# Performance work log

Measured on AMD Instinct MI355X. Metric: run time of the kernel, lower is better.

## Reference

```python
import jax, jax.numpy as jnp
import numpy as np

N, E, IN, HID, OUT, H, NCLS = 20000, 320000, 128, 32, 8, 8, 10

def _ln(x, g, b, eps=1e-5):
    mu = x.mean(-1, keepdims=True)
    var = ((x - mu) ** 2).mean(-1, keepdims=True)
    return g * (x - mu) / jnp.sqrt(var + eps) + b

def _gelu(x):
    return jax.nn.gelu(x, approximate=False)

def _tconv(x, src, dst, Wq, bq, Wk, bk, Wv, bv, Ws, bs, heads):
    # PyG TransformerConv, concat=True, root_weight=True, lin_beta is None
    n = x.shape[0]
    C = Wq.shape[1] // heads
    q = (x @ Wq + bq).reshape(n, heads, C)
    k = (x @ Wk + bk).reshape(n, heads, C)
    v = (x @ Wv + bv).reshape(n, heads, C)
    logits = (q[dst] * k[src]).sum(-1) / jnp.sqrt(jnp.asarray(C, x.dtype))  # [E,H]
    m = jax.lax.stop_gradient(jax.ops.segment_max(logits, dst, num_segments=n))
    e = jnp.exp(logits - m[dst])
    denom = jax.ops.segment_sum(e, dst, num_segments=n)
    alpha = e / (denom[dst] + 1e-16)  # per-target-node edge softmax
    agg = jax.ops.segment_sum(alpha[:, :, None] * v[src], dst, num_segments=n)
    out = agg.reshape(n, heads * C) + x @ Ws + bs
    return out, alpha

def _forward(src, dst, x,
             c1_Wq, c1_bq, c1_Wk, c1_bk, c1_Wv, c1_bv, c1_Ws, c1_bs,
             c2_Wq, c2_bq, c2_Wk, c2_bk, c2_Wv, c2_bv, c2_Ws, c2_bs,
             c3_Wq, c3_bq, c3_Wk, c3_bk, c3_Wv, c3_bv, c3_Ws, c3_bs,
             c4_Wq, c4_bq, c4_Wk, c4_bk, c4_Wv, c4_bv, c4_Ws, c4_bs,
             n1_g, n1_b, n2_g, n2_b, n3_g, n3_b, n4_g, n4_b,
             fc_W, fc_b):
    h1 = _ln(_gelu(_tconv(x, src, dst, c1_Wq, c1_bq, c1_Wk, c1_bk, c1_Wv, c1_bv, c1_Ws, c1_bs, H)[0]), n1_g, n1_b)
    h2_raw, attn = _tconv(h1, src, dst, c2_Wq, c2_bq, c2_Wk, c2_bk, c2_Wv, c2_bv, c2_Ws, c2_bs, H)
    h2 = _ln(_gelu(h2_raw), n2_g, n2_b)
    h3 = _ln(_gelu(_tconv(h2, src, dst, c3_Wq, c3_bq, c3_Wk, c3_bk, c3_Wv, c3_bv, c3_Ws, c3_bs, H)[0]), n3_g, n3_b)
    h4 = _ln(_gelu(_tconv(h3, src, dst, c4_Wq, c4_bq, c4_Wk, c4_bk, c4_Wv, c4_bv, c4_Ws, c4_bs, 1)[0]), n4_g, n4_b)
    x_out = h2 @ fc_W + fc_b
    return x_out, h4, attn

def setup_inputs() -> dict:
    key = jax.random.key(0)
    ks = iter(jax.random.split(key, 64))
    def p(shape, s=0.05):
        return jax.random.normal(next(ks), shape, dtype=jnp.float32) * s
    inp = {}
    inp['x'] = jax.random.normal(next(ks), (N, IN), dtype=jnp.float32)
    inp['edge_index'] = jax.random.randint(next(ks), (2, E), 0, N, dtype=jnp.int32)
    dims = [('c1', IN, H * HID), ('c2', H * HID, H * OUT), ('c3', H * OUT, H * HID), ('c4', H * HID, IN)]
    for name, di, do in dims:
        for w in ['Wq', 'Wk', 'Wv', 'Ws']:
            inp[name + '_' + w] = p((di, do))
        for bnm in ['bq', 'bk', 'bv', 'bs']:
            inp[name + '_' + bnm] = jnp.zeros((do,), jnp.float32)
    for nm, d in [('n1', H * HID), ('n2', H * OUT), ('n3', H * HID), ('n4', IN)]:
        inp[nm + '_g'] = jnp.ones((d,), jnp.float32)
        inp[nm + '_b'] = jnp.zeros((d,), jnp.float32)
    inp['fc_W'] = p((H * OUT, NCLS))
    inp['fc_b'] = jnp.zeros((NCLS,), jnp.float32)
    return inp

def reference(x, edge_index,
              c1_Wq, c1_bq, c1_Wk, c1_bk, c1_Wv, c1_bv, c1_Ws, c1_bs,
              c2_Wq, c2_bq, c2_Wk, c2_bk, c2_Wv, c2_bv, c2_Ws, c2_bs,
              c3_Wq, c3_bq, c3_Wk, c3_bk, c3_Wv, c3_bv, c3_Ws, c3_bs,
              c4_Wq, c4_bq, c4_Wk, c4_bk, c4_Wv, c4_bv, c4_Ws, c4_bs,
              n1_g, n1_b, n2_g, n2_b, n3_g, n3_b, n4_g, n4_b,
              fc_W, fc_b):
    src, dst = edge_index[0], edge_index[1]
    return _forward(src, dst, x,
                    c1_Wq, c1_bq, c1_Wk, c1_bk, c1_Wv, c1_bv, c1_Ws, c1_bs,
                    c2_Wq, c2_bq, c2_Wk, c2_bk, c2_Wv, c2_bv, c2_Ws, c2_bs,
                    c3_Wq, c3_bq, c3_Wk, c3_bk, c3_Wv, c3_bv, c3_Ws, c3_bs,
                    c4_Wq, c4_bq, c4_Wk, c4_bk, c4_Wv, c4_bv, c4_Ws, c4_bs,
                    n1_g, n1_b, n2_g, n2_b, n3_g, n3_b, n4_g, n4_b,
                    fc_W, fc_b)
```

## Files before the change

kernel.cpp:

```cpp
#include <hip/hip_runtime.h>
#include <hip/hip_bf16.h>
#include <math.h>

#define NN 20000
#define MP 20032
#define NE 320000

typedef __hip_bfloat16 bf16;
typedef __attribute__((ext_vector_type(8))) short short8v;
typedef __attribute__((ext_vector_type(4))) short short4v;
typedef __attribute__((ext_vector_type(4))) float f32x4;

__device__ __forceinline__ float b2f(bf16 v){ return __bfloat162float(v); }
__device__ __forceinline__ bf16 f2b(float v){ return __float2bfloat16(v); }
__device__ __forceinline__ float bfbits(short s){
  return __uint_as_float(((unsigned)(unsigned short)s) << 16);
}
__device__ __forceinline__ int clampi(int v, int lo, int hi){ return v < lo ? lo : (v > hi ? hi : v); }
__device__ __forceinline__ void stv(bf16* p, float v){ *p = f2b(v); }
__device__ __forceinline__ void stv(float* p, float v){ *p = v; }
__device__ __forceinline__ float ldv(const bf16* p){ return b2f(*p); }
__device__ __forceinline__ float ldv(const float* p){ return *p; }

__device__ __forceinline__ float fast_erf(float x){
  float ax = fabsf(x);
  float t = __builtin_amdgcn_rcpf(1.f + 0.3275911f*ax);
  float p = ((((1.061405429f*t - 1.453152027f)*t + 1.421413741f)*t
              - 0.284496736f)*t + 0.254829592f)*t;
  float y = 1.f - p*__expf(-ax*ax);
  return copysignf(y, x);
}
__device__ __forceinline__ float gelu(float x){
  return 0.5f*x*(1.f + fast_erf(x*0.70710678118654752f));
}

template<int CPL>
__device__ __forceinline__ void ldrow(const bf16* p, float* o){
  if constexpr (CPL == 16){
    short8v v0 = *reinterpret_cast<const short8v*>(p);
    short8v v1 = *reinterpret_cast<const short8v*>(p + 8);
#pragma unroll
    for (int j = 0; j < 8; j++){ o[j] = bfbits(v0[j]); o[8+j] = bfbits(v1[j]); }
  } else if constexpr (CPL == 8){
    short8v v = *reinterpret_cast<const short8v*>(p);
#pragma unroll
    for (int j = 0; j < 8; j++) o[j] = bfbits(v[j]);
  } else {
    short4v v = *reinterpret_cast<const short4v*>(p);
#pragma unroll
    for (int j = 0; j < 4; j++) o[j] = bfbits(v[j]);
  }
}
template<int CPL>
__device__ __forceinline__ void ldrowT(const bf16* p, float* o){ ldrow<CPL>(p, o); }
template<int CPL>
__device__ __forceinline__ void ldrowT(const float* p, float* o){
#pragma unroll
  for (int j = 0; j < CPL; j += 4){
    float4 v = *reinterpret_cast<const float4*>(p + j);
    o[j] = v.x; o[j+1] = v.y; o[j+2] = v.z; o[j+3] = v.w;
  }
}

__device__ __forceinline__ short8v ldA8(const bf16* p){
  return *reinterpret_cast<const short8v*>(p);
}
__device__ __forceinline__ short8v ldA8(const float* p){
  float4 a0 = *reinterpret_cast<const float4*>(p);
  float4 a1 = *reinterpret_cast<const float4*>(p + 4);
  short8v r;
  bf16 b;
  b = f2b(a0.x); r[0] = *(const short*)&b;
  b = f2b(a0.y); r[1] = *(const short*)&b;
  b = f2b(a0.z); r[2] = *(const short*)&b;
  b = f2b(a0.w); r[3] = *(const short*)&b;
  b = f2b(a1.x); r[4] = *(const short*)&b;
  b = f2b(a1.y); r[5] = *(const short*)&b;
  b = f2b(a1.z); r[6] = *(const short*)&b;
  b = f2b(a1.w); r[7] = *(const short*)&b;
  return r;
}

__global__ void fill_k(float* __restrict__ out, int n, float val){
  int i = blockIdx.x*blockDim.x + threadIdx.x;
  if (i < n) out[i] = val;
}

struct PackArgs {
  const float* w[16];
  unsigned long long off[16];
  int K[16];
  int D[16];
};
__global__ void pack_all(PackArgs pa, bf16* __restrict__ out){
  int wi = blockIdx.y;
  int K = pa.K[wi], D = pa.D[wi];
  int i = blockIdx.x*256 + threadIdx.x;
  if (i >= K*D) return;
  int j = i & 7, l = (i >> 3) & 63;
  int TG = D >> 4;
  int tg = (i >> 9) % TG, s = (i >> 9) / TG;
  int k = s*32 + (l >> 4)*8 + j, n = tg*16 + (l & 15);
  out[pa.off[wi] + i] = f2b(pa.w[wi][(size_t)k*D + n]);
}

template<typename AT, typename TS>
__global__ void gemm_qkvs(const AT* __restrict__ X,
    const short8v* __restrict__ WQ, const short8v* __restrict__ WK,
    const short8v* __restrict__ WV, const short8v* __restrict__ WS,
    const float* __restrict__ bQ, const float* __restrict__ bK,
    const float* __restrict__ bV, const float* __restrict__ bS,
    bf16* __restrict__ Qo, bf16* __restrict__ Ko, bf16* __restrict__ Vo,
    TS* __restrict__ So,
    int K, int TG, int ldQ, int ldKV, int ldS, int MstoreS){
  int w = threadIdx.x >> 6, lane = threadIdx.x & 63;
  int n0 = blockIdx.x*64;
  size_t m0 = (size_t)blockIdx.y*64 + w*16;
  int lr = lane & 15, lk = lane >> 4;
  int ar = clampi((int)(m0 + lr), 0, NN-1);
  const AT* xp = X + (size_t)ar*K + lk*8;
  size_t wo = ((size_t)(n0 >> 4))*64 + lane;
  f32x4 acc[4][4];
#pragma unroll
  for (int j = 0; j < 4; j++)
#pragma unroll
    for (int t = 0; t < 4; t++) acc[j][t] = f32x4{0,0,0,0};
  int steps = K >> 5;
  for (int s = 0; s < steps; s++){
    short8v a = ldA8(xp + s*32);
    size_t ro = wo + (size_t)s*TG*64;
#pragma unroll
    for (int t = 0; t < 4; t++){
      size_t idx = ro + t*64;
      acc[0][t] = __builtin_amdgcn_mfma_f32_16x16x32_bf16(a, WQ[idx], acc[0][t], 0, 0, 0);
      acc[1][t] = __builtin_amdgcn_mfma_f32_16x16x32_bf16(a, WK[idx], acc[1][t], 0, 0, 0);
      acc[2][t] = __builtin_amdgcn_mfma_f32_16x16x32_bf16(a, WV[idx], acc[2][t], 0, 0, 0);
      acc[3][t] = __builtin_amdgcn_mfma_f32_16x16x32_bf16(a, WS[idx], acc[3][t], 0, 0, 0);
    }
  }
#pragma unroll
  for (int t = 0; t < 4; t++){
    int col = n0 + t*16 + lr;
    float b0 = bQ[col], b1 = bK[col], b2 = bV[col], b3 = bS[col];
#pragma unroll
    for (int r = 0; r < 4; r++){
      size_t row = m0 + lk*4 + r;
      Qo[row*(size_t)ldQ  + col] = f2b(acc[0][t][r] + b0);
      Ko[row*(size_t)ldKV + col] = f2b(acc[1][t][r] + b1);
      Vo[row*(size_t)ldKV + col] = f2b(acc[2][t][r] + b2);
      if ((int)row < MstoreS) stv(&So[row*(size_t)ldS + col], acc[3][t][r] + b3);
    }
  }
}

__global__ void count_k(const int* __restrict__ ei, int* __restrict__ cnt, int E){
  int e = blockIdx.x*blockDim.x + threadIdx.x;
  if (e < E){
    int d = clampi(ei[E + e], 0, NN-1);
    atomicAdd(&cnt[d], 1);
  }
}

__global__ void exscan_k(const int* __restrict__ cnt, int* __restrict__ off,
                         int* __restrict__ cur, int n){
  __shared__ int wtot[16];
  __shared__ int carrysh;
  int tid = threadIdx.x, lane = tid & 63, w = tid >> 6;
  if (tid == 0) carrysh = 0;
  __syncthreads();
  for (int base = 0; base < n; base += 1024){
    int i = base + tid;
    int v = (i < n) ? cnt[i] : 0;
    int s = v;
#pragma unroll
    for (int d = 1; d < 64; d <<= 1){
      int t = __shfl_up(s, d);
      if (lane >= d) s += t;
    }
    if (lane == 63) wtot[w] = s;
    __syncthreads();
    int woff = 0;
    for (int j = 0; j < w; j++) woff += wtot[j];
    int c = carrysh;
    if (i < n){ int val = c + woff + s - v; off[i] = val; cur[i] = val; }
    __syncthreads();
    if (tid == 1023) carrysh = c + woff + s;
    __syncthreads();
  }
  if (threadIdx.x == 0) off[n] = carrysh;
}

__global__ void scatter_k(const int* __restrict__ ei, int* __restrict__ cur,
                          int* __restrict__ perm, int* __restrict__ srcs, int E){
  int e = blockIdx.x*blockDim.x + threadIdx.x;
  if (e >= E) return;
  int s = clampi(ei[e], 0, NN-1);
  int d = clampi(ei[E + e], 0, NN-1);
  int p = atomicAdd(&cur[d], 1);
  if (p >= 0 && p < E){ perm[p] = e; srcs[p] = s; }
}

template<int D, int H, typename TO>
__global__ void fused_attn(const bf16* __restrict__ Q, const bf16* __restrict__ KV,
                           const int* __restrict__ srcs, const int* __restrict__ offs,
                           TO* __restrict__ Xout, int ldO,
                           const float* __restrict__ G, const float* __restrict__ Bt,
                           bf16* __restrict__ LOG, const int* __restrict__ perm,
                           float* __restrict__ attn_out, float scale){
  constexpr int CPL = D/16;
  constexpr int LPH = 16/H;
  int node = blockIdx.x*4 + (threadIdx.x >> 6);
  if (node >= NN) return;
  int lane = threadIdx.x & 63;
  int hl = lane & 15;
  int slot = lane >> 4;
  float q[CPL];
  {
    float tmp[CPL];
    ldrow<CPL>(Q + (size_t)node*D + hl*CPL, tmp);
#pragma unroll
    for (int j = 0; j < CPL; j++) q[j] = tmp[j] * scale;
  }
  float den = 0.f;
  float acc[CPL];
#pragma unroll
  for (int j = 0; j < CPL; j++) acc[j] = 0.f;
  int s0 = offs[node], e0 = offs[node+1];

  float kA[CPL], vA[CPL], kB[CPL], vB[CPL];
  auto LD = [&](int i, float* k, float* v){
    int sc = (i < e0) ? srcs[i] : 0;
    const bf16* base = KV + (size_t)sc*(2*D) + hl*CPL;
    ldrow<CPL>(base,     k);
    ldrow<CPL>(base + D, v);
  };
  auto PROC = [&](int i, const float* k, const float* v){
    float t = 0.f;
#pragma unroll
    for (int j = 0; j < CPL; j++) t += q[j]*k[j];
#pragma unroll
    for (int o = 1; o < LPH; o <<= 1) t += __shfl_xor(t, o);
    bool val = i < e0;
    if (LOG && val && ((hl & (LPH-1)) == 0)) LOG[(size_t)i*H + hl/LPH] = f2b(t);
    float pe = val ? __expf(t) : 0.f;
    den += pe;
#pragma unroll
    for (int j = 0; j < CPL; j++) acc[j] += pe*v[j];
  };

  int iA = s0 + slot;
  int iters = (e0 - s0 + 3) >> 2;
  LD(iA, kA, vA);
  for (int it = 0; it < iters; it += 2){
    LD(iA + 4, kB, vB);
    PROC(iA, kA, vA);
    LD(iA + 8, kA, vA);
    PROC(iA + 4, kB, vB);
    iA += 8;
  }
  den += __shfl_xor(den, 16);
  den += __shfl_xor(den, 32);
#pragma unroll
  for (int j = 0; j < CPL; j++){
    acc[j] += __shfl_xor(acc[j], 16);
    acc[j] += __shfl_xor(acc[j], 32);
  }
  float inv = 1.f/(den + 1e-16f);

  {
    float sk[CPL];
    ldrowT<CPL>(Xout + (size_t)node*ldO + hl*CPL, sk);
    float v[CPL]; float s = 0.f;
#pragma unroll
    for (int j = 0; j < CPL; j++){
      float ge = gelu(sk[j] + acc[j]*inv);
      v[j] = ge; s += ge;
    }
#pragma unroll
    for (int o = 1; o < 16; o <<= 1) s += __shfl_xor(s, o);
    float mu = s * (1.f/D);
    float qv = 0.f;
#pragma unroll
    for (int j = 0; j < CPL; j++){ float d2 = v[j]-mu; qv += d2*d2; }
#pragma unroll
    for (int o = 1; o < 16; o <<= 1) qv += __shfl_xor(qv, o);
    float lni = 1.f / sqrtf(qv*(1.f/D) + 1e-5f);
    if (slot == 0){
      TO* oo = Xout + (size_t)node*ldO + hl*CPL;
#pragma unroll
      for (int j = 0; j < CPL; j++){
        int c = hl*CPL + j;
        stv(&oo[j], G[c]*(v[j]-mu)*lni + Bt[c]);
      }
    }
  }

  if (attn_out){
    asm volatile("s_waitcnt vmcnt(0)" ::: "memory");
    int total = (e0 - s0) * H;
    int it2 = (total + 63) >> 6;
    for (int b = 0; b < it2; b++){
      int idx = b*64 + lane;
      int h = idx & (H-1);
      float dh = __shfl(den, h*LPH);
      if (idx < total){
        int pos = s0 + (idx >> 3);
        float lg = b2f(LOG[(size_t)pos*H + h]);
        attn_out[(size_t)perm[pos]*H + h] = __expf(lg)/(dh + 1e-16f);
      }
    }
  }
}

__global__ void fc_k(const bf16* __restrict__ X, const float* __restrict__ W,
                     const float* __restrict__ B, float* __restrict__ Out,
                     int K, int D){
  int m = blockIdx.x*4 + (threadIdx.x >> 6);
  int lane = threadIdx.x & 63;
  if (m >= NN || lane >= D) return;
  float acc = B[lane];
  for (int k = 0; k < K; k++) acc += b2f(X[(size_t)m*K + k]) * W[(size_t)k*D + lane];
  Out[(size_t)m*D + lane] = acc;
}

extern "C" void kernel_launch(void* const* d_in, const int* in_sizes, int n_in,
                              void* d_out, int out_size, void* d_ws, size_t ws_size,
                              hipStream_t stream){
  int code = 0;
  if (n_in != 44) code = 100;
  else {
    const int wsz[4] = {32768,16384,16384,32768};
    const int bsz[4] = {256,64,256,128};
    bool ok = in_sizes[0] == NN*128 && in_sizes[1] == 2*NE
           && in_sizes[42] == 640 && in_sizes[43] == 10;
    for (int l = 0; l < 4 && ok; l++){
      for (int j = 0; j < 4; j++)
        ok = ok && in_sizes[2+l*8+j] == wsz[l] && in_sizes[2+l*8+4+j] == bsz[l];
      ok = ok && in_sizes[34+2*l] == bsz[l] && in_sizes[35+2*l] == bsz[l];
    }
    if (!ok) code = 140;
  }
  if (code){
    fill_k<<<((size_t)out_size+255)/256, 256, 0, stream>>>((float*)d_out, out_size, (float)code);
    return;
  }

  const float* x = (const float*)d_in[0];
  const int*   ei = (const int*)d_in[1];
  const float *W[4][4], *Bw[4][4], *lng[4], *lnb[4];
  for (int l = 0; l < 4; l++){
    for (int j = 0; j < 4; j++){
      W[l][j]  = (const float*)d_in[2 + l*8 + j];
      Bw[l][j] = (const float*)d_in[2 + l*8 + 4 + j];
    }
    lng[l] = (const float*)d_in[34 + 2*l];
    lnb[l] = (const float*)d_in[35 + 2*l];
  }
  const float* fcW = (const float*)d_in[42];
  const float* fcB = (const float*)d_in[43];

  char* ws = (char*)d_ws;
  size_t o = 0;
  auto alloc = [&](size_t bytes)->void*{ void* p = ws + o; o += (bytes + 255)/256*256; return p; };
  bf16* Hb   = (bf16*)alloc((size_t)MP*256*2);
  bf16* H2b  = (bf16*)alloc((size_t)MP*64*2);
  bf16* Qb   = (bf16*)alloc((size_t)MP*256*2);
  bf16* KVb  = (bf16*)alloc((size_t)MP*512*2);
  bf16* LOG  = (bf16*)alloc((size_t)NE*8*2);
  int* OFFS  = (int*)alloc((size_t)(NN+1)*4);
  int* CNT   = (int*)alloc((size_t)(NN+1)*4);
  int* CURS  = (int*)alloc((size_t)(NN+1)*4);
  int* PERM  = (int*)alloc((size_t)NE*4);
  int* SRCS  = (int*)alloc((size_t)(NE+16)*4);
  bf16* WPK  = (bf16*)alloc((size_t)393216*2);
  size_t need = o;

  float* out_x  = (float*)d_out;
  float* out_h4 = out_x + (size_t)NN*10;
  float* out_at = out_h4 + (size_t)NN*128;

  if (ws_size < need){
    fill_k<<<((size_t)out_size+255)/256, 256, 0, stream>>>((float*)d_out, out_size, 160.0f);
    return;
  }

  const int KD[4] = {128,256,64,256};
  const int DD[4] = {256,64,256,128};
  PackArgs pa;
  bf16* Wp[4][4];
  {
    size_t off = 0;
    for (int l = 0; l < 4; l++)
      for (int j = 0; j < 4; j++){
        int idx = l*4 + j;
        pa.w[idx] = W[l][j];
        pa.off[idx] = off;
        pa.K[idx] = KD[l];
        pa.D[idx] = DD[l];
        Wp[l][j] = WPK + off;
        off += (size_t)KD[l]*DD[l];
      }
  }
  pack_all<<<dim3(128,16),256,0,stream>>>(pa, WPK);

  hipMemsetAsync(CNT, 0, (size_t)NN*4, stream);
  count_k<<<NE/256, 256, 0, stream>>>(ei, CNT, NE);
  exscan_k<<<1, 1024, 0, stream>>>(CNT, OFFS, CURS, NN);
  scatter_k<<<NE/256, 256, 0, stream>>>(ei, CURS, PERM, SRCS, NE);

  const float s32  = 0.1767766952966369f;
  const float s8   = 0.3535533905932738f;
  const float s128 = 0.0883883476483184f;
  const dim3 g64(1, MP/64), g128(2, MP/64), g256(4, MP/64);

  gemm_qkvs<float,bf16><<<g256,256,0,stream>>>(x,
      (const short8v*)Wp[0][0], (const short8v*)Wp[0][1],
      (const short8v*)Wp[0][2], (const short8v*)Wp[0][3],
      Bw[0][0], Bw[0][1], Bw[0][2], Bw[0][3],
      Qb, KVb, KVb + 256, Hb, 128, 16, 256, 512, 256, MP);
  fused_attn<256,8,bf16><<<NN/4,256,0,stream>>>(Qb, KVb, SRCS, OFFS, Hb, 256,
      lng[0], lnb[0], nullptr, nullptr, nullptr, s32);

  gemm_qkvs<bf16,bf16><<<g64,256,0,stream>>>(Hb,
      (const short8v*)Wp[1][0], (const short8v*)Wp[1][1],
      (const short8v*)Wp[1][2], (const short8v*)Wp[1][3],
      Bw[1][0], Bw[1][1], Bw[1][2], Bw[1][3],
      Qb, KVb, KVb + 64, H2b, 256, 4, 64, 128, 64, MP);
  fused_attn<64,8,bf16><<<NN/4,256,0,stream>>>(Qb, KVb, SRCS, OFFS, H2b, 64,
      lng[1], lnb[1], LOG, PERM, out_at, s8);

  fc_k<<<NN/4,256,0,stream>>>(H2b, fcW, fcB, out_x, 64, 10);

  gemm_qkvs<bf16,bf16><<<g256,256,0,stream>>>(H2b,
      (const short8v*)Wp[2][0], (const short8v*)Wp[2][1],
      (const short8v*)Wp[2][2], (const short8v*)Wp[2][3],
      Bw[2][0], Bw[2][1], Bw[2][2], Bw[2][3],
      Qb, KVb, KVb + 256, Hb, 64, 16, 256, 512, 256, MP);
  fused_attn<256,8,bf16><<<NN/4,256,0,stream>>>(Qb, KVb, SRCS, OFFS, Hb, 256,
      lng[2], lnb[2], nullptr, nullptr, nullptr, s32);

  gemm_qkvs<bf16,float><<<g128,256,0,stream>>>(Hb,
      (const short8v*)Wp[3][0], (const short8v*)Wp[3][1],
      (const short8v*)Wp[3][2], (const short8v*)Wp[3][3],
      Bw[3][0], Bw[3][1], Bw[3][2], Bw[3][3],
      Qb, KVb, KVb + 128, out_h4, 256, 8, 128, 256, 128, NN);
  fused_attn<128,1,float><<<NN/4,256,0,stream>>>(Qb, KVb, SRCS, OFFS, out_h4, 128,
      lng[3], lnb[3], nullptr, nullptr, nullptr, s128);
}
```

Baseline: 340.6 us.

## Split wide attention layers into head-group blocks with separate GELU+LayerNorm pass

For the two 256-wide TransformerConv layers, the attention aggregation is split across a second grid dimension of 4 head groups. Each wave now handles 64 channels (4 per lane) instead of 256, which cuts registers per lane and raises occupancy and parallelism. GELU and LayerNorm, which need the whole row, move into a separate gelu_ln kernel, at the cost of an extra launch and an extra read/write of the hidden buffer. The edge loop in fused_attn is also changed from a two-buffer unrolled prefetch to a simpler single-step prefetch with register rotation.

New measurement: 349.6 us. 1.03x slower.

```diff
diff --git a/kernel.cpp b/kernel.cpp
--- a/kernel.cpp
+++ b/kernel.cpp
@@ -30,7 +30,7 @@
   float y = 1.f - p*__expf(-ax*ax);
   return copysignf(y, x);
 }
-__device__ __forceinline__ float gelu(float x){
+__device__ __forceinline__ float gelu_f(float x){
   return 0.5f*x*(1.f + fast_erf(x*0.70710678118654752f));
 }
 
@@ -200,6 +200,108 @@
   if (p >= 0 && p < E){ perm[p] = e; srcs[p] = s; }
 }
 
+template<int D, int H, int NHG>
+__global__ void attn_hg(const bf16* __restrict__ Q, const bf16* __restrict__ KV,
+                        const int* __restrict__ srcs, const int* __restrict__ offs,
+                        bf16* __restrict__ Xout, float scale){
+  constexpr int DG  = D/NHG;
+  constexpr int CPL = DG/16;
+  constexpr int LPH = (D/H)/CPL;
+  int node = blockIdx.x*4 + (threadIdx.x >> 6);
+  if (node >= NN) return;
+  int cb = blockIdx.y*DG;
+  int lane = threadIdx.x & 63;
+  int hl = lane & 15;
+  int slot = lane >> 4;
+  float q[CPL];
+  {
+    float tmp[CPL];
+    ldrow<CPL>(Q + (size_t)node*D + cb + hl*CPL, tmp);
+#pragma unroll
+    for (int j = 0; j < CPL; j++) q[j] = tmp[j] * scale;
+  }
+  float den = 0.f;
+  float acc[CPL];
+#pragma unroll
+  for (int j = 0; j < CPL; j++) acc[j] = 0.f;
+  int s0 = offs[node], e0 = offs[node+1];
+  int i = s0 + slot;
+  bool vcur = i < e0;
+  int sc = vcur ? srcs[i] : 0;
+  float kc[CPL], vc[CPL];
+  {
+    const bf16* base = KV + (size_t)sc*(2*D) + cb + hl*CPL;
+    ldrow<CPL>(base, kc); ldrow<CPL>(base + D, vc);
+  }
+  int iters = (e0 - s0 + 3) >> 2;
+  for (int it = 0; it < iters; ++it){
+    int inext = i + 4;
+    bool vnxt = inext < e0;
+    int sn = vnxt ? srcs[inext] : 0;
+    float kn[CPL], vn[CPL];
+    {
+      const bf16* base = KV + (size_t)sn*(2*D) + cb + hl*CPL;
+      ldrow<CPL>(base, kn); ldrow<CPL>(base + D, vn);
+    }
+    float t = 0.f;
+#pragma unroll
+    for (int j = 0; j < CPL; j++) t += q[j]*kc[j];
+#pragma unroll
+    for (int o = 1; o < LPH; o <<= 1) t += __shfl_xor(t, o);
+    float pe = vcur ? __expf(t) : 0.f;
+    den += pe;
+#pragma unroll
+    for (int j = 0; j < CPL; j++) acc[j] += pe*vc[j];
+    vcur = vnxt; i = inext;
+#pragma unroll
+    for (int j = 0; j < CPL; j++){ kc[j] = kn[j]; vc[j] = vn[j]; }
+  }
+  den += __shfl_xor(den, 16);
+  den += __shfl_xor(den, 32);
+#pragma unroll
+  for (int j = 0; j < CPL; j++){
+    acc[j] += __shfl_xor(acc[j], 16);
+    acc[j] += __shfl_xor(acc[j], 32);
+  }
+  float inv = 1.f/(den + 1e-16f);
+  if (slot == 0){
+    bf16* oo = Xout + (size_t)node*D + cb + hl*CPL;
+#pragma unroll
+    for (int j = 0; j < CPL; j++) oo[j] = f2b(b2f(oo[j]) + acc[j]*inv);
+  }
+}
+
+template<int CPL>
+__global__ void gelu_ln(bf16* __restrict__ X, const float* __restrict__ G,
+                        const float* __restrict__ Bt){
+  int node = blockIdx.x*4 + (threadIdx.x >> 6);
+  if (node >= NN) return;
+  constexpr int D = CPL*64;
+  int lane = threadIdx.x & 63;
+  bf16* xr = X + (size_t)node*D + lane*CPL;
+  float v[CPL]; float s = 0.f;
+  {
+    float tmp[CPL];
+    ldrow<CPL>(xr, tmp);
+#pragma unroll
+    for (int j = 0; j < CPL; j++){ float ge = gelu_f(tmp[j]); v[j] = ge; s += ge; }
+  }
+#pragma unroll
+  for (int off = 1; off < 64; off <<= 1) s += __shfl_xor(s, off);
+  float mu = s * (1.f/D);
+  float q = 0.f;
+#pragma unroll
+  for (int j = 0; j < CPL; j++){ float d = v[j]-mu; q += d*d; }
+#pragma unroll
+  for (int off = 1; off < 64; off <<= 1) q += __shfl_xor(q, off);
+  float inv = 1.f / sqrtf(q*(1.f/D) + 1e-5f);
+#pragma unroll
+  for (int j = 0; j < CPL; j++){
+    int c = lane*CPL + j;
+    xr[j] = f2b(G[c]*(v[j]-mu)*inv + Bt[c]);
+  }
+}
+
 template<int D, int H, typename TO>
 __global__ void fused_attn(const bf16* __restrict__ Q, const bf16* __restrict__ KV,
                            const int* __restrict__ srcs, const int* __restrict__ offs,
@@ -226,37 +328,37 @@
 #pragma unroll
   for (int j = 0; j < CPL; j++) acc[j] = 0.f;
   int s0 = offs[node], e0 = offs[node+1];
-
-  float kA[CPL], vA[CPL], kB[CPL], vB[CPL];
-  auto LD = [&](int i, float* k, float* v){
-    int sc = (i < e0) ? srcs[i] : 0;
+  int i = s0 + slot;
+  bool vcur = i < e0;
+  int sc = vcur ? srcs[i] : 0;
+  float kc[CPL], vc[CPL];
+  {
     const bf16* base = KV + (size_t)sc*(2*D) + hl*CPL;
-    ldrow<CPL>(base,     k);
-    ldrow<CPL>(base + D, v);
-  };
-  auto PROC = [&](int i, const float* k, const float* v){
+    ldrow<CPL>(base, kc); ldrow<CPL>(base + D, vc);
+  }
+  int iters = (e0 - s0 + 3) >> 2;
+  for (int it = 0; it < iters; ++it){
+    int inext = i + 4;
+    bool vnxt = inext < e0;
+    int sn = vnxt ? srcs[inext] : 0;
+    float kn[CPL], vn[CPL];
+    {
+      const bf16* base = KV + (size_t)sn*(2*D) + hl*CPL;
+      ldrow<CPL>(base, kn); ldrow<CPL>(base + D, vn);
+    }
     float t = 0.f;
 #pragma unroll
-    for (int j = 0; j < CPL; j++) t += q[j]*k[j];
+    for (int j = 0; j < CPL; j++) t += q[j]*kc[j];
 #pragma unroll
     for (int o = 1; o < LPH; o <<= 1) t += __shfl_xor(t, o);
-    bool val = i < e0;
-    if (LOG && val && ((hl & (LPH-1)) == 0)) LOG[(size_t)i*H + hl/LPH] = f2b(t);
-    float pe = val ? __expf(t) : 0.f;
+    if (LOG && vcur && ((hl & (LPH-1)) == 0)) LOG[(size_t)i*H + hl/LPH] = f2b(t);
+    float pe = vcur ? __expf(t) : 0.f;
     den += pe;
 #pragma unroll
-    for (int j = 0; j < CPL; j++) acc[j] += pe*v[j];
-  };
-
-  int iA = s0 + slot;
-  int iters = (e0 - s0 + 3) >> 2;
-  LD(iA, kA, vA);
-  for (int it = 0; it < iters; it += 2){
-    LD(iA + 4, kB, vB);
-    PROC(iA, kA, vA);
-    LD(iA + 8, kA, vA);
-    PROC(iA + 4, kB, vB);
-    iA += 8;
+    for (int j = 0; j < CPL; j++) acc[j] += pe*vc[j];
+    vcur = vnxt; i = inext;
+#pragma unroll
+    for (int j = 0; j < CPL; j++){ kc[j] = kn[j]; vc[j] = vn[j]; }
   }
   den += __shfl_xor(den, 16);
   den += __shfl_xor(den, 32);
@@ -273,7 +375,7 @@
     float v[CPL]; float s = 0.f;
 #pragma unroll
     for (int j = 0; j < CPL; j++){
-      float ge = gelu(sk[j] + acc[j]*inv);
+      float ge = gelu_f(sk[j] + acc[j]*inv);
       v[j] = ge; s += ge;
     }
 #pragma unroll
@@ -418,8 +520,8 @@
       (const short8v*)Wp[0][2], (const short8v*)Wp[0][3],
       Bw[0][0], Bw[0][1], Bw[0][2], Bw[0][3],
       Qb, KVb, KVb + 256, Hb, 128, 16, 256, 512, 256, MP);
-  fused_attn<256,8,bf16><<<NN/4,256,0,stream>>>(Qb, KVb, SRCS, OFFS, Hb, 256,
-      lng[0], lnb[0], nullptr, nullptr, nullptr, s32);
+  attn_hg<256,8,4><<<dim3(NN/4,4),256,0,stream>>>(Qb, KVb, SRCS, OFFS, Hb, s32);
+  gelu_ln<4><<<NN/4,256,0,stream>>>(Hb, lng[0], lnb[0]);
 
   gemm_qkvs<bf16,bf16><<<g64,256,0,stream>>>(Hb,
       (const short8v*)Wp[1][0], (const short8v*)Wp[1][1],
@@ -436,8 +538,8 @@
       (const short8v*)Wp[2][2], (const short8v*)Wp[2][3],
       Bw[2][0], Bw[2][1], Bw[2][2], Bw[2][3],
       Qb, KVb, KVb + 256, Hb, 64, 16, 256, 512, 256, MP);
-  fused_attn<256,8,bf16><<<NN/4,256,0,stream>>>(Qb, KVb, SRCS, OFFS, Hb, 256,
-      lng[2], lnb[2], nullptr, nullptr, nullptr, s32);
+  attn_hg<256,8,4><<<dim3(NN/4,4),256,0,stream>>>(Qb, KVb, SRCS, OFFS, Hb, s32);
+  gelu_ln<4><<<NN/4,256,0,stream>>>(Hb, lng[2], lnb[2]);
 
   gemm_qkvs<bf16,float><<<g128,256,0,stream>>>(Hb,
       (const short8v*)Wp[3][0], (const short8v*)Wp[3][1],
```
